# Performance work log

Measured on AMD Instinct MI355X. Metric: run time of the kernel, lower is better.

## Reference

```python
import jax, jax.numpy as jnp
import numpy as np

B, T, C, H = 4, 2048, 768, 12
HS = C // H

def setup_inputs() -> dict:
    key = jax.random.key(0)
    ks = jax.random.split(key, 5)
    s = 0.02
    return {
        "x": jax.random.normal(ks[0], (B, T, C), jnp.float32),
        "W_attn": jax.random.normal(ks[1], (C, 3 * C), jnp.float32) * s,
        "b_attn": jnp.zeros((3 * C,), jnp.float32),
        "W_proj": jax.random.normal(ks[2], (C, C), jnp.float32) * s,
        "b_proj": jnp.zeros((C,), jnp.float32),
    }

def reference(x, W_attn, b_attn, W_proj, b_proj):
    Bz, Tz, Cz = x.shape
    qkv = x @ W_attn + b_attn                       # [B,T,3C]
    q, k, v = jnp.split(qkv, 3, axis=-1)
    # [B,T,C] -> [B,H,T,HS]
    def heads(t):
        return t.reshape(Bz, Tz, H, HS).transpose(0, 2, 1, 3)
    q, k, v = heads(q), heads(k), heads(v)
    scale = 1.0 / jnp.sqrt(jnp.asarray(HS, x.dtype))
    att = jnp.einsum("bhqd,bhkd->bhqk", q, k) * scale  # [B,H,T,T]
    causal = jnp.tril(jnp.ones((Tz, Tz), bool))
    att = jnp.where(causal[None, None], att, -jnp.inf)
    att = jax.nn.softmax(att, axis=-1)
    y = jnp.einsum("bhqk,bhkd->bhqd", att, v)       # [B,H,T,HS]
    y = y.transpose(0, 2, 1, 3).reshape(Bz, Tz, Cz)
    return y @ W_proj + b_proj
```

## Files before the change

kernel.cpp:

```cpp
#include <hip/hip_runtime.h>
#include <hip/hip_bf16.h>


typedef short s16x8 __attribute__((ext_vector_type(8)));
typedef float f32x4 __attribute__((ext_vector_type(4)));
typedef unsigned short u16x4 __attribute__((ext_vector_type(4)));
typedef unsigned short u16x8 __attribute__((ext_vector_type(8)));

#define MFMA16 __builtin_amdgcn_mfma_f32_16x16x32_bf16

__device__ __forceinline__ unsigned short f2bf(float f) {
    __hip_bfloat16 h = __float2bfloat16(f);
    return *reinterpret_cast<unsigned short*>(&h);
}

__device__ __forceinline__ void gload16(const unsigned short* g, unsigned short* l) {
    __builtin_amdgcn_global_load_lds(
        (__attribute__((address_space(1))) void*)(const void*)g,
        (__attribute__((address_space(3))) void*)l, 16, 0, 0);
}

__global__ __launch_bounds__(256) void cvt_f32_bf16(
    const float* __restrict__ src, unsigned short* __restrict__ dst, int n4)
{
    int i = blockIdx.x * 256 + threadIdx.x;
    if (i >= n4) return;
    float4 v = reinterpret_cast<const float4*>(src)[i];
    u16x4 o = { f2bf(v.x), f2bf(v.y), f2bf(v.z), f2bf(v.w) };
    reinterpret_cast<u16x4*>(dst)[i] = o;
}

__global__ __launch_bounds__(256) void cvt_transpose(
    const float* __restrict__ src, unsigned short* __restrict__ dst, int R, int C)
{
    __shared__ unsigned short tile[32][33];
    const int c0 = blockIdx.x * 32, r0 = blockIdx.y * 32;
    const int tx = threadIdx.x & 31, ty = threadIdx.x >> 5;
#pragma unroll
    for (int j = 0; j < 32; j += 8)
        tile[ty + j][tx] = f2bf(src[(size_t)(r0 + ty + j) * C + c0 + tx]);
    __syncthreads();
#pragma unroll
    for (int j = 0; j < 32; j += 8)
        dst[(size_t)(c0 + ty + j) * R + r0 + tx] = tile[tx][ty + j];
}

template<bool SCALEQ, bool OUT_BF16>
__global__ __launch_bounds__(256, 2) void gemm_bt(
    const unsigned short* __restrict__ A, const unsigned short* __restrict__ Bt,
    const float* __restrict__ bias, void* __restrict__ Cout,
    int M, int N, int K)
{
    __shared__ unsigned short lds_a[128 * 64];
    __shared__ unsigned short lds_b[128 * 64];

    const int tid = threadIdx.x, lane = tid & 63, w = tid >> 6;
    const int wr = w >> 1, wc = w & 1;
    const int lr = lane & 15, lg = lane >> 4;

    const int nbx = gridDim.x;
    const int bid = blockIdx.x + nbx * blockIdx.y;
    const int cpx = (nbx * gridDim.y) >> 3;
    const int swz = (bid & 7) * cpx + (bid >> 3);
    const int m0 = (swz / nbx) * 128, n0 = (swz % nbx) * 128;

    f32x4 acc[4][4];
#pragma unroll
    for (int mi = 0; mi < 4; ++mi)
#pragma unroll
        for (int ni = 0; ni < 4; ++ni)
            acc[mi][ni] = f32x4{0.f, 0.f, 0.f, 0.f};

    const int srow = 8 * w + (lane >> 3);
    const int sslot = ((lane & 7) ^ (lane >> 3)) * 8;
    const unsigned short* Ap = A  + (size_t)(m0 + srow) * K + sslot;
    const unsigned short* Bp = Bt + (size_t)(n0 + srow) * K + sslot;
    unsigned short* la = lds_a + w * 512;
    unsigned short* lb = lds_b + w * 512;

    for (int k0 = 0; k0 < K; k0 += 64) {
#pragma unroll
        for (int p = 0; p < 4; ++p) {
            gload16(Ap + (size_t)(32 * p) * K + k0, la + 2048 * p);
            gload16(Bp + (size_t)(32 * p) * K + k0, lb + 2048 * p);
        }
        __syncthreads();

#pragma unroll
        for (int kh = 0; kh < 2; ++kh) {
            s16x8 af[4], bfr[4];
#pragma unroll
            for (int mi = 0; mi < 4; ++mi) {
                const int row = wr * 64 + mi * 16 + lr;
                af[mi] = *reinterpret_cast<const s16x8*>(
                    &lds_a[row * 64 + ((kh * 32 + lg * 8) ^ ((row & 7) << 3))]);
            }
#pragma unroll
            for (int ni = 0; ni < 4; ++ni) {
                const int row = wc * 64 + ni * 16 + lr;
                bfr[ni] = *reinterpret_cast<const s16x8*>(
                    &lds_b[row * 64 + ((kh * 32 + lg * 8) ^ ((row & 7) << 3))]);
            }
#pragma unroll
            for (int mi = 0; mi < 4; ++mi)
#pragma unroll
                for (int ni = 0; ni < 4; ++ni)
                    acc[mi][ni] = MFMA16(af[mi], bfr[ni], acc[mi][ni], 0, 0, 0);
        }
        __syncthreads();
    }

#pragma unroll
    for (int ni = 0; ni < 4; ++ni) {
        int col = n0 + wc * 64 + ni * 16 + lr;
        float bs = bias[col];
        float scq = (SCALEQ && col < 768) ? 0.18033688011112042f : 1.0f;
#pragma unroll
        for (int mi = 0; mi < 4; ++mi)
#pragma unroll
            for (int r = 0; r < 4; ++r) {
                int row = m0 + wr * 64 + mi * 16 + lg * 4 + r;
                float v = (acc[mi][ni][r] + bs) * scq;
                if (OUT_BF16)
                    ((unsigned short*)Cout)[(size_t)row * N + col] = f2bf(v);
                else
                    ((float*)Cout)[(size_t)row * N + col] = v;
            }
    }
}

__global__ __launch_bounds__(256, 4) void attn_fwd(
    const unsigned short* __restrict__ qkv, unsigned short* __restrict__ att)
{
    __shared__ unsigned short lds_k[64 * 72];
    __shared__ unsigned short lds_v[64 * 72];
    __shared__ unsigned short lds_p[4][32 * 72];

    const int tid = threadIdx.x, lane = tid & 63, w = tid >> 6;
    const int lr = lane & 15, lg = lane >> 4;
    const int bh = blockIdx.x;
    const int qt = 15 - blockIdx.y;
    const int b = bh / 12, h = bh % 12;
    const size_t bT = (size_t)b * 2048;
    const int wq = qt * 128 + w * 32;

    s16x8 qf[2][2];
#pragma unroll
    for (int mi = 0; mi < 2; ++mi) {
        const size_t qoff = (bT + wq + mi * 16 + lr) * 2304 + h * 64 + lg * 8;
        qf[mi][0] = *reinterpret_cast<const s16x8*>(qkv + qoff);
        qf[mi][1] = *reinterpret_cast<const s16x8*>(qkv + qoff + 32);
    }

    f32x4 o[2][4];
    f32x4 lsum[2];
#pragma unroll
    for (int mi = 0; mi < 2; ++mi) {
        lsum[mi] = f32x4{0.f, 0.f, 0.f, 0.f};
#pragma unroll
        for (int dt = 0; dt < 4; ++dt) o[mi][dt] = f32x4{0.f, 0.f, 0.f, 0.f};
    }

    const int ksr = tid >> 2, ksc = (tid & 3) * 16;
    const unsigned short* kbase = qkv + (bT + ksr) * 2304 + 768 + h * 64 + ksc;
    unsigned short* kdst = &lds_k[ksr * 72 + ksc];
    const int vkp = tid >> 3, vdb = (tid & 7) * 8;
    const unsigned short* vbase = qkv + (bT + 2 * vkp) * 2304 + 1536 + h * 64 + vdb;

    const int nkt = 2 * (qt + 1);

    u16x8 kr0 = *reinterpret_cast<const u16x8*>(kbase);
    u16x8 kr1 = *reinterpret_cast<const u16x8*>(kbase + 8);
    u16x8 vr0 = *reinterpret_cast<const u16x8*>(vbase);
    u16x8 vr1 = *reinterpret_cast<const u16x8*>(vbase + 2304);

    for (int kt = 0; kt < nkt; ++kt) {
        const int kv0 = kt * 64;
        *reinterpret_cast<u16x8*>(kdst)     = kr0;
        *reinterpret_cast<u16x8*>(kdst + 8) = kr1;
#pragma unroll
        for (int j = 0; j < 8; ++j) {
            const int d = vdb + j;
            unsigned pk = (unsigned)vr0[j] | ((unsigned)vr1[j] << 16);
            *reinterpret_cast<unsigned*>(
                &lds_v[d * 72 + ((2 * vkp) ^ (((d >> 3) & 7) << 3))]) = pk;
        }
        __syncthreads();

        {
            const int ktn = (kt + 1 < nkt) ? kt + 1 : kt;
            const size_t off = (size_t)(ktn * 64) * 2304;
            kr0 = *reinterpret_cast<const u16x8*>(kbase + off);
            kr1 = *reinterpret_cast<const u16x8*>(kbase + off + 8);
            vr0 = *reinterpret_cast<const u16x8*>(vbase + off);
            vr1 = *reinterpret_cast<const u16x8*>(vbase + off + 2304);
        }

        if (kv0 <= wq + 31) {
            f32x4 sf[2][4];
#pragma unroll
            for (int mi = 0; mi < 2; ++mi)
#pragma unroll
                for (int n = 0; n < 4; ++n) sf[mi][n] = f32x4{0.f, 0.f, 0.f, 0.f};
            __builtin_amdgcn_s_setprio(1);
#pragma unroll
            for (int kk = 0; kk < 2; ++kk)
#pragma unroll
                for (int n = 0; n < 4; ++n) {
                    s16x8 kf = *reinterpret_cast<const s16x8*>(
                        &lds_k[(n * 16 + lr) * 72 + kk * 32 + lg * 8]);
                    sf[0][n] = MFMA16(kf, qf[0][kk], sf[0][n], 0, 0, 0);
                    sf[1][n] = MFMA16(kf, qf[1][kk], sf[1][n], 0, 0, 0);
                }
            __builtin_amdgcn_s_setprio(0);

            if (kv0 + 63 > wq) {
#pragma unroll
                for (int mi = 0; mi < 2; ++mi)
#pragma unroll
                    for (int n = 0; n < 4; ++n)
#pragma unroll
                        for (int r = 0; r < 4; ++r) {
                            int key = kv0 + n * 16 + 4 * lg + r;
                            int qrow = wq + mi * 16 + lr;
                            if (key > qrow) sf[mi][n][r] = -1.0e30f;
                        }
            }

#pragma unroll
            for (int mi = 0; mi < 2; ++mi)
#pragma unroll
                for (int n = 0; n < 4; ++n) {
                    f32x4 p;
#pragma unroll
                    for (int r = 0; r < 4; ++r) p[r] = __builtin_amdgcn_exp2f(sf[mi][n][r]);
                    lsum[mi] += p;
                    u16x4 pk = { f2bf(p[0]), f2bf(p[1]), f2bf(p[2]), f2bf(p[3]) };
                    *reinterpret_cast<u16x4*>(
                        &lds_p[w][(mi * 16 + lr) * 72 + n * 16 + 4 * lg]) = pk;
                }

            __builtin_amdgcn_s_setprio(1);
#pragma unroll
            for (int kk = 0; kk < 2; ++kk) {
                s16x8 pf0 = *reinterpret_cast<const s16x8*>(
                    &lds_p[w][lr * 72 + kk * 32 + lg * 8]);
                s16x8 pf1 = *reinterpret_cast<const s16x8*>(
                    &lds_p[w][(16 + lr) * 72 + kk * 32 + lg * 8]);
#pragma unroll
                for (int dt = 0; dt < 4; ++dt) {
                    const int vrow = dt * 16 + lr;
                    s16x8 vf = *reinterpret_cast<const s16x8*>(
                        &lds_v[vrow * 72 + ((kk * 32 + lg * 8) ^ (((vrow >> 3) & 7) << 3))]);
                    o[0][dt] = MFMA16(pf0, vf, o[0][dt], 0, 0, 0);
                    o[1][dt] = MFMA16(pf1, vf, o[1][dt], 0, 0, 0);
                }
            }
            __builtin_amdgcn_s_setprio(0);
        }
        __syncthreads();
    }

    float inv[2];
#pragma unroll
    for (int mi = 0; mi < 2; ++mi) {
        float s = lsum[mi][0] + lsum[mi][1] + lsum[mi][2] + lsum[mi][3];
        s += __shfl_xor(s, 16);
        s += __shfl_xor(s, 32);
        inv[mi] = 1.0f / s;
    }

#pragma unroll
    for (int mi = 0; mi < 2; ++mi)
#pragma unroll
        for (int dt = 0; dt < 4; ++dt)
#pragma unroll
            for (int r = 0; r < 4; ++r) {
                int qrow = wq + mi * 16 + 4 * lg + r;
                float sc = __shfl(inv[mi], 4 * lg + r);
                att[(bT + qrow) * 768 + h * 64 + dt * 16 + lr] = f2bf(o[mi][dt][r] * sc);
            }
}

extern "C" void kernel_launch(void* const* d_in, const int* in_sizes, int n_in,
                              void* d_out, int out_size, void* d_ws, size_t ws_size,
                              hipStream_t stream) {
    const float* x      = (const float*)d_in[0];
    const float* W_attn = (const float*)d_in[1];
    const float* b_attn = (const float*)d_in[2];
    const float* W_proj = (const float*)d_in[3];
    const float* b_proj = (const float*)d_in[4];

    unsigned short* ws    = (unsigned short*)d_ws;
    unsigned short* x_bf  = ws;
    unsigned short* wa_t  = x_bf + 6291456;
    unsigned short* wp_t  = wa_t + 1769472;
    unsigned short* qkv   = wp_t + 589824;
    unsigned short* att   = qkv + 18874368;

    cvt_f32_bf16<<<6144, 256, 0, stream>>>(x, x_bf, 6291456 / 4);
    cvt_transpose<<<dim3(72, 24), 256, 0, stream>>>(W_attn, wa_t, 768, 2304);
    cvt_transpose<<<dim3(24, 24), 256, 0, stream>>>(W_proj, wp_t, 768, 768);

    gemm_bt<true , true ><<<dim3(18, 64), 256, 0, stream>>>(x_bf, wa_t, b_attn, qkv, 8192, 2304, 768);
    attn_fwd<<<dim3(48, 16), 256, 0, stream>>>(qkv, att);
    gemm_bt<false, false><<<dim3(6, 64), 256, 0, stream>>>(att, wp_t, b_proj, d_out, 8192, 768, 768);
}
```

Before: 225.3 us.

## Load K fragments into registers, double-buffer V in LDS, stage output stores

```diff
diff --git a/kernel.cpp b/kernel.cpp
--- a/kernel.cpp
+++ b/kernel.cpp
@@ -129,11 +129,10 @@
     }
 }
 
-__global__ __launch_bounds__(256, 4) void attn_fwd(
+__global__ __launch_bounds__(256, 3) void attn_fwd(
     const unsigned short* __restrict__ qkv, unsigned short* __restrict__ att)
 {
-    __shared__ unsigned short lds_k[64 * 72];
-    __shared__ unsigned short lds_v[64 * 72];
+    __shared__ unsigned short lds_v[2][64 * 72];
     __shared__ unsigned short lds_p[4][32 * 72];
 
     const int tid = threadIdx.x, lane = tid & 63, w = tid >> 6;
@@ -161,58 +160,68 @@
         for (int dt = 0; dt < 4; ++dt) o[mi][dt] = f32x4{0.f, 0.f, 0.f, 0.f};
     }
 
-    const int ksr = tid >> 2, ksc = (tid & 3) * 16;
-    const unsigned short* kbase = qkv + (bT + ksr) * 2304 + 768 + h * 64 + ksc;
-    unsigned short* kdst = &lds_k[ksr * 72 + ksc];
+    const unsigned short* kptr = qkv + (bT + lr) * 2304 + 768 + h * 64 + lg * 8;
     const int vkp = tid >> 3, vdb = (tid & 7) * 8;
-    const unsigned short* vbase = qkv + (bT + 2 * vkp) * 2304 + 1536 + h * 64 + vdb;
+    const unsigned short* vptr = qkv + (bT + 2 * vkp) * 2304 + 1536 + h * 64 + vdb;
+    const int vkx = (2 * vkp);
 
     const int nkt = 2 * (qt + 1);
-
-    u16x8 kr0 = *reinterpret_cast<const u16x8*>(kbase);
-    u16x8 kr1 = *reinterpret_cast<const u16x8*>(kbase + 8);
-    u16x8 vr0 = *reinterpret_cast<const u16x8*>(vbase);
-    u16x8 vr1 = *reinterpret_cast<const u16x8*>(vbase + 2304);
-
-    for (int kt = 0; kt < nkt; ++kt) {
-        const int kv0 = kt * 64;
-        *reinterpret_cast<u16x8*>(kdst)     = kr0;
-        *reinterpret_cast<u16x8*>(kdst + 8) = kr1;
+    const int ktmax = (wq + 31) >> 6;
+    const size_t TSTEP = (size_t)64 * 2304;
+
+    {
+        u16x8 v0 = *reinterpret_cast<const u16x8*>(vptr);
+        u16x8 v1 = *reinterpret_cast<const u16x8*>(vptr + 2304);
 #pragma unroll
         for (int j = 0; j < 8; ++j) {
             const int d = vdb + j;
-            unsigned pk = (unsigned)vr0[j] | ((unsigned)vr1[j] << 16);
+            unsigned pk = (unsigned)v0[j] | ((unsigned)v1[j] << 16);
             *reinterpret_cast<unsigned*>(
-                &lds_v[d * 72 + ((2 * vkp) ^ (((d >> 3) & 7) << 3))]) = pk;
-        }
+                &lds_v[0][d * 72 + (vkx ^ (((d >> 3) & 7) << 3))]) = pk;
+        }
+    }
+    s16x8 kfc[4][2];
+#pragma unroll
+    for (int n = 0; n < 4; ++n)
+#pragma unroll
+        for (int kk = 0; kk < 2; ++kk)
+            kfc[n][kk] = *reinterpret_cast<const s16x8*>(kptr + (size_t)(n * 16) * 2304 + kk * 32);
+
+    for (int kt = 0; kt < nkt; ++kt) {
         __syncthreads();
-
-        {
-            const int ktn = (kt + 1 < nkt) ? kt + 1 : kt;
-            const size_t off = (size_t)(ktn * 64) * 2304;
-            kr0 = *reinterpret_cast<const u16x8*>(kbase + off);
-            kr1 = *reinterpret_cast<const u16x8*>(kbase + off + 8);
-            vr0 = *reinterpret_cast<const u16x8*>(vbase + off);
-            vr1 = *reinterpret_cast<const u16x8*>(vbase + off + 2304);
-        }
-
-        if (kv0 <= wq + 31) {
+        const int kv0 = kt * 64;
+
+        u16x8 nv0, nv1;
+        const bool havev = (kt + 1 < nkt);
+        if (havev) {
+            const unsigned short* vp = vptr + (size_t)(kt + 1) * TSTEP;
+            nv0 = *reinterpret_cast<const u16x8*>(vp);
+            nv1 = *reinterpret_cast<const u16x8*>(vp + 2304);
+        }
+        s16x8 kfn[4][2];
+        const bool havek = (kt + 1 <= ktmax);
+        if (havek) {
+            const unsigned short* kp = kptr + (size_t)(kt + 1) * TSTEP;
+#pragma unroll
+            for (int n = 0; n < 4; ++n)
+#pragma unroll
+                for (int kk = 0; kk < 2; ++kk)
+                    kfn[n][kk] = *reinterpret_cast<const s16x8*>(kp + (size_t)(n * 16) * 2304 + kk * 32);
+        }
+
+        if (kt <= ktmax) {
             f32x4 sf[2][4];
 #pragma unroll
             for (int mi = 0; mi < 2; ++mi)
 #pragma unroll
                 for (int n = 0; n < 4; ++n) sf[mi][n] = f32x4{0.f, 0.f, 0.f, 0.f};
-            __builtin_amdgcn_s_setprio(1);
 #pragma unroll
             for (int kk = 0; kk < 2; ++kk)
 #pragma unroll
                 for (int n = 0; n < 4; ++n) {
-                    s16x8 kf = *reinterpret_cast<const s16x8*>(
-                        &lds_k[(n * 16 + lr) * 72 + kk * 32 + lg * 8]);
-                    sf[0][n] = MFMA16(kf, qf[0][kk], sf[0][n], 0, 0, 0);
-                    sf[1][n] = MFMA16(kf, qf[1][kk], sf[1][n], 0, 0, 0);
+                    sf[0][n] = MFMA16(kfc[n][kk], qf[0][kk], sf[0][n], 0, 0, 0);
+                    sf[1][n] = MFMA16(kfc[n][kk], qf[1][kk], sf[1][n], 0, 0, 0);
                 }
-            __builtin_amdgcn_s_setprio(0);
 
             if (kv0 + 63 > wq) {
 #pragma unroll
@@ -240,7 +249,7 @@
                         &lds_p[w][(mi * 16 + lr) * 72 + n * 16 + 4 * lg]) = pk;
                 }
 
-            __builtin_amdgcn_s_setprio(1);
+            const unsigned short* vb = lds_v[kt & 1];
 #pragma unroll
             for (int kk = 0; kk < 2; ++kk) {
                 s16x8 pf0 = *reinterpret_cast<const s16x8*>(
@@ -251,14 +260,30 @@
                 for (int dt = 0; dt < 4; ++dt) {
                     const int vrow = dt * 16 + lr;
                     s16x8 vf = *reinterpret_cast<const s16x8*>(
-                        &lds_v[vrow * 72 + ((kk * 32 + lg * 8) ^ (((vrow >> 3) & 7) << 3))]);
+                        &vb[vrow * 72 + ((kk * 32 + lg * 8) ^ (((vrow >> 3) & 7) << 3))]);
                     o[0][dt] = MFMA16(pf0, vf, o[0][dt], 0, 0, 0);
                     o[1][dt] = MFMA16(pf1, vf, o[1][dt], 0, 0, 0);
                 }
             }
-            __builtin_amdgcn_s_setprio(0);
-        }
-        __syncthreads();
+        }
+
+        if (havev) {
+            unsigned short* vdst = lds_v[(kt + 1) & 1];
+#pragma unroll
+            for (int j = 0; j < 8; ++j) {
+                const int d = vdb + j;
+                unsigned pk = (unsigned)nv0[j] | ((unsigned)nv1[j] << 16);
+                *reinterpret_cast<unsigned*>(
+                    &vdst[d * 72 + (vkx ^ (((d >> 3) & 7) << 3))]) = pk;
+            }
+        }
+        if (havek) {
+#pragma unroll
+            for (int n = 0; n < 4; ++n)
+#pragma unroll
+                for (int kk = 0; kk < 2; ++kk)
+                    kfc[n][kk] = kfn[n][kk];
+        }
     }
 
     float inv[2];
@@ -273,13 +298,22 @@
 #pragma unroll
     for (int mi = 0; mi < 2; ++mi)
 #pragma unroll
-        for (int dt = 0; dt < 4; ++dt)
+        for (int dt = 0; dt < 4; ++dt) {
 #pragma unroll
             for (int r = 0; r < 4; ++r) {
-                int qrow = wq + mi * 16 + 4 * lg + r;
                 float sc = __shfl(inv[mi], 4 * lg + r);
-                att[(bT + qrow) * 768 + h * 64 + dt * 16 + lr] = f2bf(o[mi][dt][r] * sc);
-            }
+                lds_p[w][(mi * 16 + 4 * lg + r) * 72 + dt * 16 + lr] =
+                    f2bf(o[mi][dt][r] * sc);
+            }
+        }
+    const int erow = lane >> 1;
+#pragma unroll
+    for (int j = 0; j < 4; ++j) {
+        const int ec = (lane & 1) + 2 * j;
+        u16x8 val = *reinterpret_cast<const u16x8*>(&lds_p[w][erow * 72 + ec * 8]);
+        *reinterpret_cast<u16x8*>(
+            &att[(bT + wq + erow) * 768 + h * 64 + ec * 8]) = val;
+    }
 }
 
 extern "C" void kernel_launch(void* const* d_in, const int* in_sizes, int n_in,
```

After: 313.6 us. 1.39x slower.
